# Performance work log

Hardware: AMD Instinct MI355X
Metric: run time of the kernel (lower is better)

Reference implementation:

```python
import jax, jax.numpy as jnp
import numpy as np
from jax import lax

INPUT_SIZE = 10
HIDDEN = 128
NUM_CLASSES = 10
B, T = 256, 512


def setup_inputs() -> dict:
    key = jax.random.key(0)
    ks = jax.random.split(key, 12)
    s = 1.0 / np.sqrt(HIDDEN)
    inp = {
        "x": jax.random.normal(ks[0], (B, T, INPUT_SIZE), dtype=jnp.float32),
        # layer 0 (input_size -> hidden), PyTorch gate order [i, f, g, o]
        "w_ih0": jax.random.uniform(ks[1], (4 * HIDDEN, INPUT_SIZE), minval=-s, maxval=s),
        "w_hh0": jax.random.uniform(ks[2], (4 * HIDDEN, HIDDEN), minval=-s, maxval=s),
        "b_ih0": jax.random.uniform(ks[3], (4 * HIDDEN,), minval=-s, maxval=s),
        "b_hh0": jax.random.uniform(ks[4], (4 * HIDDEN,), minval=-s, maxval=s),
        # layer 1 (hidden -> hidden)
        "w_ih1": jax.random.uniform(ks[5], (4 * HIDDEN, HIDDEN), minval=-s, maxval=s),
        "w_hh1": jax.random.uniform(ks[6], (4 * HIDDEN, HIDDEN), minval=-s, maxval=s),
        "b_ih1": jax.random.uniform(ks[7], (4 * HIDDEN,), minval=-s, maxval=s),
        "b_hh1": jax.random.uniform(ks[8], (4 * HIDDEN,), minval=-s, maxval=s),
        # final classifier
        "fc_w": jax.random.uniform(ks[9], (NUM_CLASSES, HIDDEN), minval=-s, maxval=s),
        "fc_b": jax.random.uniform(ks[10], (NUM_CLASSES,), minval=-s, maxval=s),
    }
    return inp


def _lstm_layer(x_seq, w_ih, w_hh, b_ih, b_hh):
    """x_seq: [B, T, D_in] -> hidden sequence [B, T, H]. PyTorch gate order i,f,g,o."""
    b = x_seq.shape[0]
    h_dim = w_hh.shape[1]
    # precompute input contribution as one big GEMM: [B, T, 4H]
    x_gates = jnp.einsum('btd,gd->btg', x_seq, w_ih) + b_ih + b_hh
    x_gates_t = jnp.swapaxes(x_gates, 0, 1)  # [T, B, 4H]

    def step(carry, xg):
        h, c = carry
        gates = xg + h @ w_hh.T  # [B, 4H]
        i, f, g, o = jnp.split(gates, 4, axis=-1)
        i = jax.nn.sigmoid(i)
        f = jax.nn.sigmoid(f)
        g = jnp.tanh(g)
        o = jax.nn.sigmoid(o)
        c_new = f * c + i * g
        h_new = o * jnp.tanh(c_new)
        return (h_new, c_new), h_new

    h0 = jnp.zeros((b, h_dim), dtype=x_seq.dtype)
    c0 = jnp.zeros((b, h_dim), dtype=x_seq.dtype)
    _, hs = lax.scan(step, (h0, c0), x_gates_t)  # hs: [T, B, H]
    return jnp.swapaxes(hs, 0, 1)  # [B, T, H]


def reference(x, w_ih0, w_hh0, b_ih0, b_hh0, w_ih1, w_hh1, b_ih1, b_hh1, fc_w, fc_b):
    h1 = _lstm_layer(x, w_ih0, w_hh0, b_ih0, b_hh0)      # [B, T, H]
    h2 = _lstm_layer(h1, w_ih1, w_hh1, b_ih1, b_hh1)     # [B, T, H]
    last = h2[:, -1, :]                                   # [B, H]
    return last @ fc_w.T + fc_b                           # [B, num_classes]
```

## Files before the change

kernel.cpp:

```cpp
#include <hip/hip_runtime.h>

#define HID   128
#define GATES 512
#define BATCH 256
#define SEQ   512
#define INSZ  10
#define MB    16
#define NBLK  (BATCH / MB)
#define NTHR  512
#define HSTR  136
#define XSTR  40
#define XCH   8
#define HCH   4
#define PCH   8

typedef _Float16 half8  __attribute__((ext_vector_type(8)));
typedef _Float16 half2v __attribute__((ext_vector_type(2)));
typedef float    floatx4 __attribute__((ext_vector_type(4)));

#define MFMA16(A, B, C) __builtin_amdgcn_mfma_f32_16x16x32_f16(A, B, C, 0, 0, 0)

#define KSIG  (-1.4426950408889634f)
#define KTAN  (-2.8853900817779268f)

__device__ __forceinline__ float sigm_pre(float a)
{
    return __builtin_amdgcn_rcpf(1.0f + __builtin_amdgcn_exp2f(a));
}
__device__ __forceinline__ float tanh_pre(float a)
{
    return __builtin_fmaf(2.0f, __builtin_amdgcn_rcpf(1.0f + __builtin_amdgcn_exp2f(a)), -1.0f);
}
__device__ __forceinline__ float tanh_plain(float c)
{
    return tanh_pre(c * KTAN);
}

__device__ __forceinline__ half8 load_wfrag(const float* rowbase, int k0, float scale)
{
    const float4* p = (const float4*)(rowbase + k0);
    float4 a = p[0], b = p[1];
    half8 r;
    r[0] = (_Float16)(a.x * scale); r[1] = (_Float16)(a.y * scale);
    r[2] = (_Float16)(a.z * scale); r[3] = (_Float16)(a.w * scale);
    r[4] = (_Float16)(b.x * scale); r[5] = (_Float16)(b.y * scale);
    r[6] = (_Float16)(b.z * scale); r[7] = (_Float16)(b.w * scale);
    return r;
}

#define XBUF_HALFS (XCH * MB * XSTR)
#define H1C_BUF_HALFS (HCH * MB * HSTR)
#define H0_OFF  20480
#define H2_OFF  34816
#define LDS_BYTES 43520

__device__ __forceinline__ int wait_flag(int* flagp, int needed, int lastf)
{
    if (lastf >= needed) return lastf;
    int f = __hip_atomic_load(flagp, __ATOMIC_RELAXED, __HIP_MEMORY_SCOPE_AGENT);
    while (f < needed) {
        __builtin_amdgcn_s_sleep(2);
        f = __hip_atomic_load(flagp, __ATOMIC_RELAXED, __HIP_MEMORY_SCOPE_AGENT);
    }
    (void)__hip_atomic_load(flagp, __ATOMIC_ACQUIRE, __HIP_MEMORY_SCOPE_AGENT);
    return f;
}

__global__ __launch_bounds__(NTHR, 2)
void lstm_fused(const float* __restrict__ x,
                const float* __restrict__ w_ih0, const float* __restrict__ w_hh0,
                const float* __restrict__ b_ih0, const float* __restrict__ b_hh0,
                const float* __restrict__ w_ih1, const float* __restrict__ w_hh1,
                const float* __restrict__ b_ih1, const float* __restrict__ b_hh1,
                const float* __restrict__ fc_w,  const float* __restrict__ fc_b,
                float* __restrict__ out, _Float16* __restrict__ h1w_all)
{
    const int tid  = threadIdx.x;
    const int lane = tid & 63;
    const int wv   = tid >> 6;
    const int m16  = lane & 15;
    const int quad = lane >> 4;
    const int col  = (wv << 4) + m16;

    const bool producer = (blockIdx.x < NBLK);
    const int  pb = producer ? blockIdx.x : blockIdx.x - NBLK;
    const int  b0 = pb * MB;

    __shared__ __align__(16) char lds[LDS_BYTES];
    _Float16* xs  = (_Float16*)lds;
    _Float16* h0s = (_Float16*)(lds + H0_OFF);
    _Float16* h1c = (_Float16*)lds;
    _Float16* h2s = (_Float16*)(lds + H2_OFF);
    float*    h2f = (float*)lds;

    _Float16* h1w = h1w_all + (size_t)pb * SEQ * MB * HID;
    int* flagp = (int*)out + pb * (MB * 10);

    const float gsc[4] = {KSIG, KSIG, KTAN, KSIG};

    if (producer) {
        half8 Whh0f[4][4];
        half8 Wih0f[4];
        float bias0[4];
#pragma unroll
        for (int g = 0; g < 4; ++g) {
            const int gr = g * HID + col;
            const float sc = gsc[g];
            bias0[g] = (b_ih0[gr] + b_hh0[gr]) * sc;
#pragma unroll
            for (int ks = 0; ks < 4; ++ks)
                Whh0f[g][ks] = load_wfrag(w_hh0 + (size_t)gr * HID, ks * 32 + quad * 8, sc);
            half8 r;
#pragma unroll
            for (int j = 0; j < 8; ++j) {
                int k = quad * 8 + j;
                r[j] = (k < INSZ) ? (_Float16)(w_ih0[gr * INSZ + k] * sc) : (_Float16)0.0f;
            }
            Wih0f[g] = r;
        }

        for (int i = tid; i < (H0_OFF + 8704) / 4; i += NTHR) ((int*)lds)[i] = 0;

        if (tid < 128) {
            const int sr = tid >> 4, mr = tid & 15;
            const float2* xp = (const float2*)(x + ((size_t)(b0 + mr) * SEQ + sr) * INSZ);
            _Float16* dst = xs + (sr * MB + mr) * XSTR;
#pragma unroll
            for (int p = 0; p < 5; ++p) {
                float2 v = xp[p];
                half2v h; h[0] = (_Float16)v.x; h[1] = (_Float16)v.y;
                *(half2v*)(dst + 2 * p) = h;
            }
        }
        __syncthreads();

        float c0[4] = {0.f, 0.f, 0.f, 0.f};
        float2 xr[5];
        floatx4 xg[4][4];

        auto xburst = [&](int base) {
            const _Float16* xb = xs + ((base >> 3) & 1) * XBUF_HALFS;
#pragma unroll
            for (int k = 0; k < 4; ++k) {
                half8 xa = *(const half8*)(xb + (((base & 7) + k) * MB + m16) * XSTR + quad * 8);
#pragma unroll
                for (int g = 0; g < 4; ++g) {
                    floatx4 a = {bias0[g], bias0[g], bias0[g], bias0[g]};
                    a = MFMA16(xa, Wih0f[g], a);
                    xg[k][g] = a;
                }
            }
        };
        xburst(0);

        for (int tc = 0; tc < SEQ; tc += 8) {
#pragma unroll
            for (int s8 = 0; s8 < 8; ++s8) {
                const int t = tc + s8;
                const int sl = s8 & 3;
                if (s8 == 0 && t + XCH < SEQ && tid < 128) {
                    const int sr = tid >> 4, mr = tid & 15;
                    const float2* xp = (const float2*)(x + ((size_t)(b0 + mr) * SEQ + (t + XCH + sr)) * INSZ);
#pragma unroll
                    for (int p = 0; p < 5; ++p) xr[p] = xp[p];
                }
                const _Float16* hb = h0s + (s8 & 1) * (MB * HSTR) + m16 * HSTR + quad * 8;
                half8 ha0 = *(const half8*)(hb);
                half8 ha1 = *(const half8*)(hb + 32);
                half8 ha2 = *(const half8*)(hb + 64);
                half8 ha3 = *(const half8*)(hb + 96);
#pragma unroll
                for (int g = 0; g < 4; ++g) {
                    floatx4 a = xg[sl][g];
                    a = MFMA16(ha0, Whh0f[g][0], a);
                    a = MFMA16(ha1, Whh0f[g][1], a);
                    a = MFMA16(ha2, Whh0f[g][2], a);
                    a = MFMA16(ha3, Whh0f[g][3], a);
                    xg[sl][g] = a;
                }
                if (s8 == 2 && t + 6 < SEQ && tid < 128) {
                    const int sr = tid >> 4, mr = tid & 15;
                    _Float16* dst = xs + (((t >> 3) + 1) & 1) * XBUF_HALFS + (sr * MB + mr) * XSTR;
#pragma unroll
                    for (int p = 0; p < 5; ++p) {
                        half2v h; h[0] = (_Float16)xr[p].x; h[1] = (_Float16)xr[p].y;
                        *(half2v*)(dst + 2 * p) = h;
                    }
                }
                _Float16* hw = h0s + ((s8 & 1) ^ 1) * (MB * HSTR);
#pragma unroll
                for (int e = 0; e < 4; ++e) {
                    float iv = sigm_pre(xg[sl][0][e]);
                    float fv = sigm_pre(xg[sl][1][e]);
                    float gv = tanh_pre(xg[sl][2][e]);
                    float ov = sigm_pre(xg[sl][3][e]);
                    c0[e] = __builtin_fmaf(fv, c0[e], iv * gv);
                    float hv = ov * tanh_plain(c0[e]);
                    _Float16 hh = (_Float16)hv;
                    const int row = quad * 4 + e;
                    hw[row * HSTR + col] = hh;
                    h1w[((size_t)t * MB + row) * HID + col] = hh;
                }
                if ((s8 == 3 || s8 == 7) && t + 4 < SEQ) xburst(t + 1);
                __syncthreads();
                if (s8 == 7 && tid == 0) {
                    __threadfence();
                    __hip_atomic_store(flagp, t + 1, __ATOMIC_RELEASE, __HIP_MEMORY_SCOPE_AGENT);
                }
            }
        }
        return;
    }

    half8 Wih1f[4][4], Whh1f[4][4];
    float bias1[4];
#pragma unroll
    for (int g = 0; g < 4; ++g) {
        const int gr = g * HID + col;
        const float sc = gsc[g];
        bias1[g] = (b_ih1[gr] + b_hh1[gr]) * sc;
#pragma unroll
        for (int ks = 0; ks < 4; ++ks) {
            Wih1f[g][ks] = load_wfrag(w_ih1 + (size_t)gr * HID, ks * 32 + quad * 8, sc);
            Whh1f[g][ks] = load_wfrag(w_hh1 + (size_t)gr * HID, ks * 32 + quad * 8, sc);
        }
    }
    for (int i = tid; i < 2176; i += NTHR) ((int*)(lds + H2_OFF))[i] = 0;

    int lastf = 0;
    lastf = wait_flag(flagp, PCH, lastf);

#pragma unroll
    for (int r = 0; r < 2; ++r) {
        const int fi = tid + NTHR * r;
        const int ef = fi * 8;
        const int ss = ef >> 11, rem = ef & 2047;
        const int mm = rem >> 7, k0 = rem & 127;
        int4 v = *(const int4*)(h1w + ef);
        *(int4*)(h1c + (ss * MB + mm) * HSTR + k0) = v;
    }
    __syncthreads();

    floatx4 pg[4][4];

    auto pburst = [&](int base) {
        const _Float16* sb = h1c + ((base >> 2) & 1) * H1C_BUF_HALFS;
#pragma unroll
        for (int k = 0; k < 4; ++k) {
            const _Float16* pp = sb + (k * MB + m16) * HSTR + quad * 8;
            half8 f0 = *(const half8*)(pp);
            half8 f1 = *(const half8*)(pp + 32);
            half8 f2 = *(const half8*)(pp + 64);
            half8 f3 = *(const half8*)(pp + 96);
#pragma unroll
            for (int g = 0; g < 4; ++g) {
                floatx4 a = {bias1[g], bias1[g], bias1[g], bias1[g]};
                a = MFMA16(f0, Wih1f[g][0], a);
                a = MFMA16(f1, Wih1f[g][1], a);
                a = MFMA16(f2, Wih1f[g][2], a);
                a = MFMA16(f3, Wih1f[g][3], a);
                pg[k][g] = a;
            }
        }
    };
    pburst(0);

    float c1[4] = {0.f, 0.f, 0.f, 0.f};
    int4 hr0, hr1;
    for (int tc = 0; tc < SEQ; tc += 4) {
#pragma unroll
        for (int s = 0; s < 4; ++s) {
            const int t = tc + s;
            if (s == 0 && t + HCH < SEQ) {
                lastf = wait_flag(flagp, t + 2 * HCH, lastf);
                const _Float16* src = h1w + (size_t)((t >> 2) + 1) * (HCH * MB * HID);
                hr0 = *(const int4*)(src + tid * 8);
                hr1 = *(const int4*)(src + (tid + NTHR) * 8);
            }
            const _Float16* h2b = h2s + (s & 1) * (MB * HSTR) + m16 * HSTR + quad * 8;
            half8 q0 = *(const half8*)(h2b);
            half8 q1 = *(const half8*)(h2b + 32);
            half8 q2 = *(const half8*)(h2b + 64);
            half8 q3 = *(const half8*)(h2b + 96);
#pragma unroll
            for (int g = 0; g < 4; ++g) {
                floatx4 a = pg[s][g];
                a = MFMA16(q0, Whh1f[g][0], a);
                a = MFMA16(q1, Whh1f[g][1], a);
                a = MFMA16(q2, Whh1f[g][2], a);
                a = MFMA16(q3, Whh1f[g][3], a);
                pg[s][g] = a;
            }
            if (s == 2 && t + 2 < SEQ) {
                _Float16* dstb = h1c + (((t >> 2) + 1) & 1) * H1C_BUF_HALFS;
                int ef = tid * 8;
                int ss = ef >> 11, rem = ef & 2047, mm = rem >> 7, k0 = rem & 127;
                *(int4*)(dstb + (ss * MB + mm) * HSTR + k0) = hr0;
                ef = (tid + NTHR) * 8;
                ss = ef >> 11; rem = ef & 2047; mm = rem >> 7; k0 = rem & 127;
                *(int4*)(dstb + (ss * MB + mm) * HSTR + k0) = hr1;
            }
            _Float16* hw2 = h2s + ((s & 1) ^ 1) * (MB * HSTR);
#pragma unroll
            for (int e = 0; e < 4; ++e) {
                float iv = sigm_pre(pg[s][0][e]);
                float fv = sigm_pre(pg[s][1][e]);
                float gv = tanh_pre(pg[s][2][e]);
                float ov = sigm_pre(pg[s][3][e]);
                c1[e] = __builtin_fmaf(fv, c1[e], iv * gv);
                float hv = ov * tanh_plain(c1[e]);
                const int row = quad * 4 + e;
                hw2[row * HSTR + col] = (_Float16)hv;
                if (t == SEQ - 1) h2f[row * 132 + col] = hv;
            }
            if (s == 3 && t + 1 < SEQ) pburst(t + 1);
            __syncthreads();
        }
    }

    if (tid < 160) {
        const int cls = tid >> 4, b = tid & 15;
        float a = fc_b[cls];
        const float* wr = fc_w + cls * HID;
#pragma unroll 8
        for (int k = 0; k < HID; ++k) a += wr[k] * h2f[b * 132 + k];
        out[(size_t)(b0 + b) * 10 + cls] = a;
    }
}

extern "C" void kernel_launch(void* const* d_in, const int* in_sizes, int n_in,
                              void* d_out, int out_size, void* d_ws, size_t ws_size,
                              hipStream_t stream) {
    (void)in_sizes; (void)n_in; (void)out_size; (void)ws_size;
    const float* x     = (const float*)d_in[0];
    const float* w_ih0 = (const float*)d_in[1];
    const float* w_hh0 = (const float*)d_in[2];
    const float* b_ih0 = (const float*)d_in[3];
    const float* b_hh0 = (const float*)d_in[4];
    const float* w_ih1 = (const float*)d_in[5];
    const float* w_hh1 = (const float*)d_in[6];
    const float* b_ih1 = (const float*)d_in[7];
    const float* b_hh1 = (const float*)d_in[8];
    const float* fc_w  = (const float*)d_in[9];
    const float* fc_b  = (const float*)d_in[10];
    float* out = (float*)d_out;
    _Float16* h1w = (_Float16*)d_ws;

    hipMemsetAsync(d_out, 0, BATCH * 10 * sizeof(float), stream);
    lstm_fused<<<2 * NBLK, NTHR, 0, stream>>>(x, w_ih0, w_hh0, b_ih0, b_hh0,
                                              w_ih1, w_hh1, b_ih1, b_hh1,
                                              fc_w, fc_b, out, h1w);
}
```

Baseline: 606.7 us.

## Spread input-gate MFMA bursts across steps and precompute pointer offsets

Replaces the periodic burst that computes input-projection gates for four future timesteps at once with a per-step computation of the gates for step t+4, issued after the activation math. This spreads the input-GEMM MFMA work evenly so each recurrent step's critical path is balanced, overlapping it with the elementwise gate work. The consumer now prefetches two chunks ahead and waits on an earlier flag, and the address arithmetic is hoisted into precomputed base pointers and swapped buffers. It adds register pressure for the extra fragments and changes the producer/consumer lag.

After: 680.1 us. 1.12x slower.

```diff
diff --git a/kernel.cpp b/kernel.cpp
--- a/kernel.cpp
+++ b/kernel.cpp
@@ -101,12 +101,13 @@
     if (producer) {
         half8 Whh0f[4][4];
         half8 Wih0f[4];
-        float bias0[4];
+        floatx4 biasv0[4];
 #pragma unroll
         for (int g = 0; g < 4; ++g) {
             const int gr = g * HID + col;
             const float sc = gsc[g];
-            bias0[g] = (b_ih0[gr] + b_hh0[gr]) * sc;
+            const float b = (b_ih0[gr] + b_hh0[gr]) * sc;
+            biasv0[g] = (floatx4){b, b, b, b};
 #pragma unroll
             for (int ks = 0; ks < 4; ++ks)
                 Whh0f[g][ks] = load_wfrag(w_hh0 + (size_t)gr * HID, ks * 32 + quad * 8, sc);
@@ -121,50 +122,54 @@
 
         for (int i = tid; i < (H0_OFF + 8704) / 4; i += NTHR) ((int*)lds)[i] = 0;
 
+        const int sr = tid >> 4, mr = tid & 15;
+        const int xdoff = (sr * MB + mr) * XSTR;
+        const float2* xgp = (const float2*)(x + ((size_t)(b0 + mr) * SEQ + sr) * INSZ);
+
         if (tid < 128) {
-            const int sr = tid >> 4, mr = tid & 15;
-            const float2* xp = (const float2*)(x + ((size_t)(b0 + mr) * SEQ + sr) * INSZ);
-            _Float16* dst = xs + (sr * MB + mr) * XSTR;
+            _Float16* dst = xs + xdoff;
 #pragma unroll
             for (int p = 0; p < 5; ++p) {
-                float2 v = xp[p];
+                float2 v = xgp[p];
                 half2v h; h[0] = (_Float16)v.x; h[1] = (_Float16)v.y;
                 *(half2v*)(dst + 2 * p) = h;
             }
         }
+        xgp += XCH * INSZ / 2;
         __syncthreads();
 
         float c0[4] = {0.f, 0.f, 0.f, 0.f};
         float2 xr[5];
         floatx4 xg[4][4];
 
-        auto xburst = [&](int base) {
-            const _Float16* xb = xs + ((base >> 3) & 1) * XBUF_HALFS;
-#pragma unroll
-            for (int k = 0; k < 4; ++k) {
-                half8 xa = *(const half8*)(xb + (((base & 7) + k) * MB + m16) * XSTR + quad * 8);
-#pragma unroll
-                for (int g = 0; g < 4; ++g) {
-                    floatx4 a = {bias0[g], bias0[g], bias0[g], bias0[g]};
-                    a = MFMA16(xa, Wih0f[g], a);
-                    xg[k][g] = a;
-                }
-            }
-        };
-        xburst(0);
+        const _Float16* xcur = xs;
+        _Float16*       xnxt = xs + XBUF_HALFS;
+        const int xb0 = m16 * XSTR + quad * 8;
+        const _Float16* h0r = h0s + m16 * HSTR + quad * 8;
+        _Float16*       h0w = h0s + (quad * 4) * HSTR + col;
+        _Float16*       h1p = h1w + (size_t)(quad * 4) * HID + col;
+
+#pragma unroll
+        for (int k = 0; k < 4; ++k) {
+            half8 xa = *(const half8*)(xcur + k * (MB * XSTR) + xb0);
+#pragma unroll
+            for (int g = 0; g < 4; ++g) {
+                floatx4 a = biasv0[g];
+                a = MFMA16(xa, Wih0f[g], a);
+                xg[k][g] = a;
+            }
+        }
 
         for (int tc = 0; tc < SEQ; tc += 8) {
 #pragma unroll
             for (int s8 = 0; s8 < 8; ++s8) {
                 const int t = tc + s8;
                 const int sl = s8 & 3;
-                if (s8 == 0 && t + XCH < SEQ && tid < 128) {
-                    const int sr = tid >> 4, mr = tid & 15;
-                    const float2* xp = (const float2*)(x + ((size_t)(b0 + mr) * SEQ + (t + XCH + sr)) * INSZ);
-#pragma unroll
-                    for (int p = 0; p < 5; ++p) xr[p] = xp[p];
-                }
-                const _Float16* hb = h0s + (s8 & 1) * (MB * HSTR) + m16 * HSTR + quad * 8;
+                if (s8 == 0 && tc + XCH < SEQ && tid < 128) {
+#pragma unroll
+                    for (int p = 0; p < 5; ++p) xr[p] = xgp[p];
+                }
+                const _Float16* hb = h0r + (s8 & 1) * (MB * HSTR);
                 half8 ha0 = *(const half8*)(hb);
                 half8 ha1 = *(const half8*)(hb + 32);
                 half8 ha2 = *(const half8*)(hb + 64);
@@ -178,16 +183,20 @@
                     a = MFMA16(ha3, Whh0f[g][3], a);
                     xg[sl][g] = a;
                 }
-                if (s8 == 2 && t + 6 < SEQ && tid < 128) {
-                    const int sr = tid >> 4, mr = tid & 15;
-                    _Float16* dst = xs + (((t >> 3) + 1) & 1) * XBUF_HALFS + (sr * MB + mr) * XSTR;
+                if (s8 == 2 && tc + XCH < SEQ && tid < 128) {
+                    _Float16* dst = xnxt + xdoff;
 #pragma unroll
                     for (int p = 0; p < 5; ++p) {
                         half2v h; h[0] = (_Float16)xr[p].x; h[1] = (_Float16)xr[p].y;
                         *(half2v*)(dst + 2 * p) = h;
                     }
                 }
-                _Float16* hw = h0s + ((s8 & 1) ^ 1) * (MB * HSTR);
+                const bool doRe = (t + 4 < SEQ);
+                half8 xa2;
+                if (doRe)
+                    xa2 = *(const half8*)(((s8 < 4) ? xcur : (const _Float16*)xnxt)
+                                          + ((s8 + 4) & 7) * (MB * XSTR) + xb0);
+                _Float16* hw = h0w + ((s8 & 1) ^ 1) * (MB * HSTR);
 #pragma unroll
                 for (int e = 0; e < 4; ++e) {
                     float iv = sigm_pre(xg[sl][0][e]);
@@ -197,28 +206,38 @@
                     c0[e] = __builtin_fmaf(fv, c0[e], iv * gv);
                     float hv = ov * tanh_plain(c0[e]);
                     _Float16 hh = (_Float16)hv;
-                    const int row = quad * 4 + e;
-                    hw[row * HSTR + col] = hh;
-                    h1w[((size_t)t * MB + row) * HID + col] = hh;
-                }
-                if ((s8 == 3 || s8 == 7) && t + 4 < SEQ) xburst(t + 1);
+                    hw[e * HSTR] = hh;
+                    h1p[(s8 * MB + e) * HID] = hh;
+                }
+                if (doRe) {
+#pragma unroll
+                    for (int g = 0; g < 4; ++g) {
+                        floatx4 a = biasv0[g];
+                        a = MFMA16(xa2, Wih0f[g], a);
+                        xg[sl][g] = a;
+                    }
+                }
                 __syncthreads();
                 if (s8 == 7 && tid == 0) {
                     __threadfence();
                     __hip_atomic_store(flagp, t + 1, __ATOMIC_RELEASE, __HIP_MEMORY_SCOPE_AGENT);
                 }
             }
+            { const _Float16* tmp = xcur; xcur = xnxt; xnxt = (_Float16*)tmp; }
+            xgp += XCH * INSZ / 2;
+            h1p += 8 * MB * HID;
         }
         return;
     }
 
     half8 Wih1f[4][4], Whh1f[4][4];
-    float bias1[4];
+    floatx4 biasv1[4];
 #pragma unroll
     for (int g = 0; g < 4; ++g) {
         const int gr = g * HID + col;
         const float sc = gsc[g];
-        bias1[g] = (b_ih1[gr] + b_hh1[gr]) * sc;
+        const float b = (b_ih1[gr] + b_hh1[gr]) * sc;
+        biasv1[g] = (floatx4){b, b, b, b};
 #pragma unroll
         for (int ks = 0; ks < 4; ++ks) {
             Wih1f[g][ks] = load_wfrag(w_ih1 + (size_t)gr * HID, ks * 32 + quad * 8, sc);
@@ -227,57 +246,65 @@
     }
     for (int i = tid; i < 2176; i += NTHR) ((int*)(lds + H2_OFF))[i] = 0;
 
+    const int ef0 = tid * 8, ef1 = (tid + NTHR) * 8;
+    const int so0 = ((ef0 >> 11) * MB + ((ef0 & 2047) >> 7)) * HSTR + (ef0 & 127);
+    const int so1 = ((ef1 >> 11) * MB + ((ef1 & 2047) >> 7)) * HSTR + (ef1 & 127);
+
     int lastf = 0;
-    lastf = wait_flag(flagp, PCH, lastf);
-
-#pragma unroll
-    for (int r = 0; r < 2; ++r) {
-        const int fi = tid + NTHR * r;
-        const int ef = fi * 8;
-        const int ss = ef >> 11, rem = ef & 2047;
-        const int mm = rem >> 7, k0 = rem & 127;
-        int4 v = *(const int4*)(h1w + ef);
-        *(int4*)(h1c + (ss * MB + mm) * HSTR + k0) = v;
+    lastf = wait_flag(flagp, 8, lastf);
+
+    {
+        int4 a0v = *(const int4*)(h1w + ef0);
+        int4 a1v = *(const int4*)(h1w + ef1);
+        *(int4*)(h1c + so0) = a0v;
+        *(int4*)(h1c + so1) = a1v;
+        const _Float16* s2 = h1w + HCH * MB * HID;
+        int4 b0v = *(const int4*)(s2 + ef0);
+        int4 b1v = *(const int4*)(s2 + ef1);
+        *(int4*)(h1c + H1C_BUF_HALFS + so0) = b0v;
+        *(int4*)(h1c + H1C_BUF_HALFS + so1) = b1v;
     }
     __syncthreads();
 
     floatx4 pg[4][4];
-
-    auto pburst = [&](int base) {
-        const _Float16* sb = h1c + ((base >> 2) & 1) * H1C_BUF_HALFS;
-#pragma unroll
-        for (int k = 0; k < 4; ++k) {
-            const _Float16* pp = sb + (k * MB + m16) * HSTR + quad * 8;
-            half8 f0 = *(const half8*)(pp);
-            half8 f1 = *(const half8*)(pp + 32);
-            half8 f2 = *(const half8*)(pp + 64);
-            half8 f3 = *(const half8*)(pp + 96);
-#pragma unroll
-            for (int g = 0; g < 4; ++g) {
-                floatx4 a = {bias1[g], bias1[g], bias1[g], bias1[g]};
-                a = MFMA16(f0, Wih1f[g][0], a);
-                a = MFMA16(f1, Wih1f[g][1], a);
-                a = MFMA16(f2, Wih1f[g][2], a);
-                a = MFMA16(f3, Wih1f[g][3], a);
-                pg[k][g] = a;
-            }
-        }
-    };
-    pburst(0);
+    const int prb = m16 * HSTR + quad * 8;
+
+#pragma unroll
+    for (int k = 0; k < 4; ++k) {
+        const _Float16* pp = h1c + k * (MB * HSTR) + prb;
+        half8 f0 = *(const half8*)(pp);
+        half8 f1 = *(const half8*)(pp + 32);
+        half8 f2 = *(const half8*)(pp + 64);
+        half8 f3 = *(const half8*)(pp + 96);
+#pragma unroll
+        for (int g = 0; g < 4; ++g) {
+            floatx4 a = biasv1[g];
+            a = MFMA16(f0, Wih1f[g][0], a);
+            a = MFMA16(f1, Wih1f[g][1], a);
+            a = MFMA16(f2, Wih1f[g][2], a);
+            a = MFMA16(f3, Wih1f[g][3], a);
+            pg[k][g] = a;
+        }
+    }
 
     float c1[4] = {0.f, 0.f, 0.f, 0.f};
     int4 hr0, hr1;
+    const _Float16* bufR = h1c + H1C_BUF_HALFS;
+    _Float16*       bufW = h1c;
+    const _Float16* h2r = h2s + m16 * HSTR + quad * 8;
+    _Float16*       h2w = h2s + (quad * 4) * HSTR + col;
+
     for (int tc = 0; tc < SEQ; tc += 4) {
 #pragma unroll
         for (int s = 0; s < 4; ++s) {
             const int t = tc + s;
-            if (s == 0 && t + HCH < SEQ) {
-                lastf = wait_flag(flagp, t + 2 * HCH, lastf);
-                const _Float16* src = h1w + (size_t)((t >> 2) + 1) * (HCH * MB * HID);
-                hr0 = *(const int4*)(src + tid * 8);
-                hr1 = *(const int4*)(src + (tid + NTHR) * 8);
-            }
-            const _Float16* h2b = h2s + (s & 1) * (MB * HSTR) + m16 * HSTR + quad * 8;
+            if (s == 0 && tc + 8 < SEQ) {
+                lastf = wait_flag(flagp, tc + 12, lastf);
+                const _Float16* src = h1w + (size_t)(tc + 8) * MB * HID;
+                hr0 = *(const int4*)(src + ef0);
+                hr1 = *(const int4*)(src + ef1);
+            }
+            const _Float16* h2b = h2r + (s & 1) * (MB * HSTR);
             half8 q0 = *(const half8*)(h2b);
             half8 q1 = *(const half8*)(h2b + 32);
             half8 q2 = *(const half8*)(h2b + 64);
@@ -291,16 +318,20 @@
                 a = MFMA16(q3, Whh1f[g][3], a);
                 pg[s][g] = a;
             }
-            if (s == 2 && t + 2 < SEQ) {
-                _Float16* dstb = h1c + (((t >> 2) + 1) & 1) * H1C_BUF_HALFS;
-                int ef = tid * 8;
-                int ss = ef >> 11, rem = ef & 2047, mm = rem >> 7, k0 = rem & 127;
-                *(int4*)(dstb + (ss * MB + mm) * HSTR + k0) = hr0;
-                ef = (tid + NTHR) * 8;
-                ss = ef >> 11; rem = ef & 2047; mm = rem >> 7; k0 = rem & 127;
-                *(int4*)(dstb + (ss * MB + mm) * HSTR + k0) = hr1;
-            }
-            _Float16* hw2 = h2s + ((s & 1) ^ 1) * (MB * HSTR);
+            if (s == 2 && tc + 8 < SEQ) {
+                *(int4*)(bufW + so0) = hr0;
+                *(int4*)(bufW + so1) = hr1;
+            }
+            const bool doRe = (t + 4 < SEQ);
+            half8 f0, f1, f2, f3;
+            if (doRe) {
+                const _Float16* pp = bufR + s * (MB * HSTR) + prb;
+                f0 = *(const half8*)(pp);
+                f1 = *(const half8*)(pp + 32);
+                f2 = *(const half8*)(pp + 64);
+                f3 = *(const half8*)(pp + 96);
+            }
+            _Float16* hw2 = h2w + ((s & 1) ^ 1) * (MB * HSTR);
 #pragma unroll
             for (int e = 0; e < 4; ++e) {
                 float iv = sigm_pre(pg[s][0][e]);
@@ -309,13 +340,23 @@
                 float ov = sigm_pre(pg[s][3][e]);
                 c1[e] = __builtin_fmaf(fv, c1[e], iv * gv);
                 float hv = ov * tanh_plain(c1[e]);
-                const int row = quad * 4 + e;
-                hw2[row * HSTR + col] = (_Float16)hv;
-                if (t == SEQ - 1) h2f[row * 132 + col] = hv;
-            }
-            if (s == 3 && t + 1 < SEQ) pburst(t + 1);
+                hw2[e * HSTR] = (_Float16)hv;
+                if (t == SEQ - 1) h2f[(quad * 4 + e) * 132 + col] = hv;
+            }
+            if (doRe) {
+#pragma unroll
+                for (int g = 0; g < 4; ++g) {
+                    floatx4 a = biasv1[g];
+                    a = MFMA16(f0, Wih1f[g][0], a);
+                    a = MFMA16(f1, Wih1f[g][1], a);
+                    a = MFMA16(f2, Wih1f[g][2], a);
+                    a = MFMA16(f3, Wih1f[g][3], a);
+                    pg[s][g] = a;
+                }
+            }
             __syncthreads();
         }
+        { const _Float16* tmp = bufR; bufR = bufW; bufW = (_Float16*)tmp; }
     }
 
     if (tid < 160) {
```
